# Kernel optimization log

Hardware: AMD Instinct MI355X
Metric: run time of the kernel (lower is better)

The kernel has to match this reference:

```python
import jax, jax.numpy as jnp
import numpy as np

ACT_BIT = 3
W_BIT = 2


def fake_quant(x, bits):
    """Symmetric uniform fake-quantization to `bits` bits (dequantized values)."""
    qmax = float((1 << (bits - 1)) - 1)
    scale = jnp.max(jnp.abs(x)) / qmax
    scale = jnp.where(scale == 0, jnp.ones_like(scale), scale)
    return jnp.clip(jnp.round(x / scale), -qmax, qmax) * scale


def setup_inputs() -> dict:
    key = jax.random.key(0)
    kA, kX, kWi, kWo = jax.random.split(key, 4)
    N, D_IN, D_H, D_OUT = 8192, 128, 64, 16
    A = jax.random.normal(kA, (N, N), dtype=jnp.float32)       # dense subgraph adjacency (binarized inside)
    X = jax.random.normal(kX, (N, D_IN), dtype=jnp.float32)    # node features
    W_in = jax.random.normal(kWi, (D_IN, D_H), dtype=jnp.float32)
    W_out = jax.random.normal(kWo, (D_H, D_OUT), dtype=jnp.float32)
    return {"A": A, "X": X, "W_in": W_in, "W_out": W_out}


def reference(A, X, W_in, W_out):
    # QGTC GCNConv_Qnt: A quantized to 1 bit, activations to act_bit, weights to w_bit.
    Aq = (A > 0).astype(A.dtype)                 # 1-bit adjacency (bit_qnt(A, 1))
    Xq = fake_quant(X, ACT_BIT)                  # X_Qnt
    Wi = fake_quant(W_in, W_BIT)                 # weight_Qnt
    Wo = fake_quant(W_out, W_BIT)
    # Layer 1: mm_v1(X, W_in) then mm_v1(A, .) with output re-quantized to act_bit
    h = Aq @ (Xq @ Wi)                           # [N, D_H]
    hq = fake_quant(h, ACT_BIT)
    # Layer 2 (output layer)
    out = Aq @ (hq @ Wo)                         # [N, D_OUT]
    return out
```

## Files before the change

### kernel.cpp

```cpp
#include <hip/hip_runtime.h>

#define NN 8192
#define DIN 128
#define DH 64
#define DOUT 16
#define KS 8

typedef _Float16 half8 __attribute__((ext_vector_type(8)));
typedef float f32x4 __attribute__((ext_vector_type(4)));

#define OFF_SC    0u
#define OFF_PART  256u
#define OFF_YT    65536u
#define OFF_RT    1114112u
#define OFF_HF    1376256u
#define OFF_BITS  3473408u
#define OFF_P1    11862016u

__device__ __forceinline__ int permk(int k) {
  int e = k & 255;
  return (k & ~255) | (((e & 3) << 6) | (e >> 2));
}

__device__ __forceinline__ float getscale(const unsigned* sc, int idx, float qmax) {
  float s = __uint_as_float(sc[idx]) / qmax;
  return (s == 0.0f) ? 1.0f : s;
}

__device__ __forceinline__ half8 expand8(unsigned bb) {
  uint4 w;
  w.x = ((bb & 1u)  ? 0x3C00u : 0u) | ((bb & 2u)   ? 0x3C000000u : 0u);
  w.y = ((bb & 4u)  ? 0x3C00u : 0u) | ((bb & 8u)   ? 0x3C000000u : 0u);
  w.z = ((bb & 16u) ? 0x3C00u : 0u) | ((bb & 32u)  ? 0x3C000000u : 0u);
  w.w = ((bb & 64u) ? 0x3C00u : 0u) | ((bb & 128u) ? 0x3C000000u : 0u);
  return __builtin_bit_cast(half8, w);
}

__global__ __launch_bounds__(256) void k_scalesbits(const float* __restrict__ A,
                                                    const float* __restrict__ X,
                                                    const float* __restrict__ Wi,
                                                    const float* __restrict__ Wo,
                                                    unsigned char* __restrict__ bits,
                                                    unsigned* part, unsigned* sc) {
  const int t = threadIdx.x, bx = blockIdx.x;
  if (bx < 4096) {
    const int lane = t & 63, warp = t >> 6;
    const size_t wbase = ((size_t)bx * 4 + warp) * 4096;
    const float4* ap = (const float4*)(A + wbase) + lane;
    unsigned char* bp = bits + (wbase >> 3);
#pragma unroll
    for (int g = 0; g < 16; ++g) {
      float4 v = ap[g * 64];
      unsigned long long m0 = __ballot(v.x > 0.0f);
      unsigned long long m1 = __ballot(v.y > 0.0f);
      unsigned long long m2 = __ballot(v.z > 0.0f);
      unsigned long long m3 = __ballot(v.w > 0.0f);
      unsigned long long lo = (lane & 1) ? m1 : m0;
      unsigned long long hi = (lane & 1) ? m3 : m2;
      unsigned long long word = (lane & 2) ? hi : lo;
      if (lane < 4) *(unsigned long long*)(bp + g * 32 + lane * 8) = word;
    }
    return;
  }
  __shared__ float red[256];
  const int b = bx - 4096;
  float m = 0.0f;
  if (b < 240) {
    for (int i = b * 256 + t; i < NN * DIN; i += 240 * 256) m = fmaxf(m, fabsf(X[i]));
  } else if (b == 240) {
    for (int i = t; i < DIN * DH; i += 256) m = fmaxf(m, fabsf(Wi[i]));
    if (t == 0) sc[3] = 0u;
  } else {
    for (int i = t; i < DH * DOUT; i += 256) m = fmaxf(m, fabsf(Wo[i]));
  }
  red[t] = m; __syncthreads();
  for (int s = 128; s > 0; s >>= 1) {
    if (t < s) red[t] = fmaxf(red[t], red[t + s]);
    __syncthreads();
  }
  if (t == 0) part[b] = __float_as_uint(red[0]);
}

__global__ __launch_bounds__(256) void k_Y(const float* __restrict__ X,
                                           const float* __restrict__ Wi,
                                           const unsigned* __restrict__ part,
                                           unsigned* sc,
                                           _Float16* __restrict__ Yb) {
  __shared__ float red[256];
  __shared__ float Xs[8][129];
  __shared__ float Ws[DIN][DH];
  const int t = threadIdx.x;
  red[t] = (t < 240) ? __uint_as_float(part[t]) : 0.0f;
  __syncthreads();
  for (int s = 128; s > 0; s >>= 1) {
    if (t < s) red[t] = fmaxf(red[t], red[t + s]);
    __syncthreads();
  }
  float sxraw = red[0];
  float sx = sxraw / 3.0f; sx = (sx == 0.0f) ? 1.0f : sx;
  float swi = __uint_as_float(part[240]); swi = (swi == 0.0f) ? 1.0f : swi;
  if (blockIdx.x == 0 && t == 0) sc[0] = __float_as_uint(sxraw);
  const int k0 = blockIdx.x * 8;
  __syncthreads();
  for (int i = t; i < 8 * DIN; i += 256) {
    int r = i >> 7, c = i & 127;
    float q = rintf(X[(size_t)(k0 + r) * DIN + c] / sx);
    Xs[r][c] = fminf(fmaxf(q, -3.0f), 3.0f);
  }
  for (int i = t; i < DIN * DH; i += 256) {
    float q = rintf(Wi[i] / swi);
    Ws[i >> 6][i & 63] = fminf(fmaxf(q, -1.0f), 1.0f);
  }
  __syncthreads();
  const int r = t & 7, jp = t >> 3, j = jp * 2;
  float a0 = 0.0f, a1 = 0.0f;
  for (int n = 0; n < DIN; ++n) {
    float xv = Xs[r][n];
    a0 = fmaf(xv, Ws[n][j], a0);
    a1 = fmaf(xv, Ws[n][j + 1], a1);
  }
  const int kp = permk(k0 + r);
  const size_t base = (size_t)(kp >> 3) * 512 + (size_t)j * 8 + (kp & 7);
  Yb[base]     = (_Float16)a0;
  Yb[base + 8] = (_Float16)a1;
}

__global__ __launch_bounds__(256) void k_gemm1(const unsigned char* __restrict__ bits,
                                               const _Float16* __restrict__ Yb,
                                               float* __restrict__ P1) {
  __shared__ __align__(16) char Ls[65536];
  const int t = threadIdx.x, lane = t & 63, warp = t >> 6;
  const int row0 = blockIdx.x * 256;
  const int split = blockIdx.y;
  const int l15 = lane & 15, lq = lane >> 4;
  const int sh8 = lq * 8;

  f32x4 acc[4][4] = {};
  const char* ysrc = (const char*)Yb + (size_t)split * 131072;
  const unsigned char* bbase = bits + split * 128;

  for (int half = 0; half < 2; ++half) {
    __syncthreads();
    {
      const uint4* src = (const uint4*)(ysrc + half * 65536) + t;
      uint4* dst = (uint4*)Ls + t;
#pragma unroll
      for (int p = 0; p < 16; ++p) dst[p * 256] = src[p * 256];
    }
    __syncthreads();
#pragma unroll
    for (int it = 0; it < 8; ++it) {
      uint2 w[4];
#pragma unroll
      for (int rt = 0; rt < 4; ++rt)
        w[rt] = *(const uint2*)(bbase +
                 (size_t)(row0 + warp * 64 + rt * 16 + l15) * 1024 + half * 64 + it * 8);
#pragma unroll
      for (int kk = 0; kk < 2; ++kk) {
        half8 bf[4];
#pragma unroll
        for (int nt = 0; nt < 4; ++nt)
          bf[nt] = *(const half8*)(&Ls[(it * 8 + kk * 4 + lq) * 1024 + (nt * 16 + l15) * 16]);
#pragma unroll
        for (int rt = 0; rt < 4; ++rt) {
          half8 af = expand8(((kk ? w[rt].y : w[rt].x) >> sh8) & 0xffu);
#pragma unroll
          for (int nt = 0; nt < 4; ++nt)
            acc[rt][nt] = __builtin_amdgcn_mfma_f32_16x16x32_f16(af, bf[nt], acc[rt][nt], 0, 0, 0);
        }
      }
    }
  }
  const int r4 = lq * 4;
#pragma unroll
  for (int rt = 0; rt < 4; ++rt) {
#pragma unroll
    for (int nt = 0; nt < 4; ++nt) {
#pragma unroll
      for (int i = 0; i < 4; ++i) {
        int rr = row0 + warp * 64 + rt * 16 + r4 + i;
        int cc = nt * 16 + l15;
        P1[((size_t)split * NN + rr) * DH + cc] = acc[rt][nt][i];
      }
    }
  }
}

__global__ __launch_bounds__(256) void k_h2(const float* __restrict__ P1,
                                            const unsigned* __restrict__ part,
                                            unsigned* sc, float* __restrict__ hf) {
  float sx = getscale(sc, 0, 3.0f);
  float swi = __uint_as_float(part[240]); swi = (swi == 0.0f) ? 1.0f : swi;
  float sxw = sx * swi;
  int idx = blockIdx.x * 256 + threadIdx.x;
  const float4* p = (const float4*)P1;
  float4 s = {0, 0, 0, 0};
#pragma unroll
  for (int sp = 0; sp < KS; ++sp) {
    float4 v = p[(size_t)sp * (NN * DH / 4) + idx];
    s.x += v.x; s.y += v.y; s.z += v.z; s.w += v.w;
  }
  s.x *= sxw; s.y *= sxw; s.z *= sxw; s.w *= sxw;
  ((float4*)hf)[idx] = s;
  float m = fmaxf(fmaxf(fabsf(s.x), fabsf(s.y)), fmaxf(fabsf(s.z), fabsf(s.w)));
  __shared__ float red[256];
  red[threadIdx.x] = m; __syncthreads();
  for (int st = 128; st > 0; st >>= 1) {
    if (threadIdx.x < st) red[threadIdx.x] = fmaxf(red[threadIdx.x], red[threadIdx.x + st]);
    __syncthreads();
  }
  if (threadIdx.x == 0) atomicMax(&sc[3], __float_as_uint(red[0]));
}

__global__ __launch_bounds__(256) void k_R(const float* __restrict__ hf,
                                           const float* __restrict__ Wo,
                                           const unsigned* __restrict__ part,
                                           const unsigned* __restrict__ sc,
                                           _Float16* __restrict__ RT) {
  __shared__ float WoS[DH][DOUT];
  float sh = getscale(sc, 3, 3.0f);
  float swo = __uint_as_float(part[241]); swo = (swo == 0.0f) ? 1.0f : swo;
  int t = threadIdx.x;
  for (int i = t; i < DH * DOUT; i += 256) {
    float q = rintf(Wo[i] / swo);
    WoS[i >> 4][i & 15] = fminf(fmaxf(q, -1.0f), 1.0f);
  }
  __syncthreads();
  int i = blockIdx.x * 16 + (t & 15), j = t >> 4;
  const float4* hp = (const float4*)(hf + (size_t)i * DH);
  float acc = 0.0f;
#pragma unroll 4
  for (int nb = 0; nb < 16; ++nb) {
    float4 h4 = hp[nb];
    float q;
    q = fminf(fmaxf(rintf(h4.x / sh), -3.0f), 3.0f); acc = fmaf(q, WoS[nb * 4 + 0][j], acc);
    q = fminf(fmaxf(rintf(h4.y / sh), -3.0f), 3.0f); acc = fmaf(q, WoS[nb * 4 + 1][j], acc);
    q = fminf(fmaxf(rintf(h4.z / sh), -3.0f), 3.0f); acc = fmaf(q, WoS[nb * 4 + 2][j], acc);
    q = fminf(fmaxf(rintf(h4.w / sh), -3.0f), 3.0f); acc = fmaf(q, WoS[nb * 4 + 3][j], acc);
  }
  RT[(size_t)j * NN + permk(i)] = (_Float16)acc;
}

__global__ __launch_bounds__(256) void k_gemm2(const unsigned char* __restrict__ bits,
                                               const _Float16* __restrict__ RT,
                                               const unsigned* __restrict__ part,
                                               const unsigned* __restrict__ sc,
                                               float* __restrict__ out) {
  __shared__ float red2[3][16][16];
  const int t = threadIdx.x, lane = t & 63, warp = t >> 6;
  const int row0 = blockIdx.x * 16;
  const int l15 = lane & 15, lq = lane >> 4;
  const int sh8 = lq * 8;

  const unsigned char* brow = bits + (size_t)(row0 + l15) * 1024 + warp * 256;
  const _Float16* rrow = RT + (size_t)l15 * NN + warp * 2048 + lq * 8;

  f32x4 acc = {};
#pragma unroll 8
  for (int it = 0; it < 32; ++it) {
    uint2 w = *(const uint2*)(brow + it * 8);
#pragma unroll
    for (int kk = 0; kk < 2; ++kk) {
      half8 af = expand8(((kk ? w.y : w.x) >> sh8) & 0xffu);
      half8 bf = *(const half8*)(rrow + it * 64 + kk * 32);
      acc = __builtin_amdgcn_mfma_f32_16x16x32_f16(af, bf, acc, 0, 0, 0);
    }
  }
  if (warp > 0) {
#pragma unroll
    for (int i = 0; i < 4; ++i) red2[warp - 1][lq * 4 + i][l15] = acc[i];
  }
  __syncthreads();
  if (warp == 0) {
    float sh = getscale(sc, 3, 3.0f);
    float swo = __uint_as_float(part[241]); swo = (swo == 0.0f) ? 1.0f : swo;
    float s = sh * swo;
#pragma unroll
    for (int i = 0; i < 4; ++i) {
      int r = lq * 4 + i;
      float v = acc[i] + red2[0][r][l15] + red2[1][r][l15] + red2[2][r][l15];
      out[(size_t)(row0 + r) * DOUT + l15] = v * s;
    }
  }
}

extern "C" void kernel_launch(void* const* d_in, const int* in_sizes, int n_in,
                              void* d_out, int out_size, void* d_ws, size_t ws_size,
                              hipStream_t stream) {
  const float* A  = (const float*)d_in[0];
  const float* X  = (const float*)d_in[1];
  const float* Wi = (const float*)d_in[2];
  const float* Wo = (const float*)d_in[3];
  char* ws = (char*)d_ws;
  unsigned* sc        = (unsigned*)(ws + OFF_SC);
  unsigned* part      = (unsigned*)(ws + OFF_PART);
  _Float16* Yb        = (_Float16*)(ws + OFF_YT);
  _Float16* RT        = (_Float16*)(ws + OFF_RT);
  float* hf           = (float*)(ws + OFF_HF);
  unsigned char* bits = (unsigned char*)(ws + OFF_BITS);
  float* P1           = (float*)(ws + OFF_P1);
  float* out          = (float*)d_out;

  k_scalesbits<<<4338, 256, 0, stream>>>(A, X, Wi, Wo, bits, part, sc);
  k_Y<<<1024, 256, 0, stream>>>(X, Wi, part, sc, Yb);
  k_gemm1<<<dim3(NN / 256, KS), 256, 0, stream>>>(bits, Yb, P1);
  k_h2<<<NN * DH / 1024, 256, 0, stream>>>(P1, part, sc, hf);
  k_R<<<NN / 16, 256, 0, stream>>>(hf, Wo, part, sc, RT);
  k_gemm2<<<NN / 16, 256, 0, stream>>>(bits, RT, part, sc, out);
}
```

Measured before the change: 127.0 us.

## Restructure pipeline into uniform 512-block kernels with atomic-free scale reductions

Rewrites all six kernels to run on a fixed grid of 512 blocks. The adjacency-binarization blocks now loop over several chunks instead of launching thousands of small blocks. The first adjacency GEMM doubles its K-split and reads Y fragments straight from global/L2 instead of staging them through 64KB of LDS. The atomicMax on the hidden-layer max is replaced by per-block partials that each consumer re-reduces, and the combined scale factors are folded into the final output. This is meant to cut launch and occupancy overhead and LDS pressure, at the cost of doubling the partial-sum buffer traffic and repeating small reductions in every block.

```diff
diff --git a/kernel.cpp b/kernel.cpp
--- a/kernel.cpp
+++ b/kernel.cpp
@@ -4,14 +4,14 @@
 #define DIN 128
 #define DH 64
 #define DOUT 16
-#define KS 8
+#define KS 16
 
 typedef _Float16 half8 __attribute__((ext_vector_type(8)));
 typedef float f32x4 __attribute__((ext_vector_type(4)));
 
-#define OFF_SC    0u
-#define OFF_PART  256u
-#define OFF_YT    65536u
+#define OFF_PART  0u
+#define OFF_PART2 2048u
+#define OFF_YB    65536u
 #define OFF_RT    1114112u
 #define OFF_HF    1376256u
 #define OFF_BITS  3473408u
@@ -22,10 +22,7 @@
   return (k & ~255) | (((e & 3) << 6) | (e >> 2));
 }
 
-__device__ __forceinline__ float getscale(const unsigned* sc, int idx, float qmax) {
-  float s = __uint_as_float(sc[idx]) / qmax;
-  return (s == 0.0f) ? 1.0f : s;
-}
+__device__ __forceinline__ float guard(float s) { return (s == 0.0f) ? 1.0f : s; }
 
 __device__ __forceinline__ half8 expand8(unsigned bb) {
   uint4 w;
@@ -36,16 +33,17 @@
   return __builtin_bit_cast(half8, w);
 }
 
-__global__ __launch_bounds__(256) void k_scalesbits(const float* __restrict__ A,
-                                                    const float* __restrict__ X,
-                                                    const float* __restrict__ Wi,
-                                                    const float* __restrict__ Wo,
-                                                    unsigned char* __restrict__ bits,
-                                                    unsigned* part, unsigned* sc) {
-  const int t = threadIdx.x, bx = blockIdx.x;
-  if (bx < 4096) {
-    const int lane = t & 63, warp = t >> 6;
-    const size_t wbase = ((size_t)bx * 4 + warp) * 4096;
+__global__ __launch_bounds__(256) void k_f0(const float* __restrict__ A,
+                                            const float* __restrict__ X,
+                                            const float* __restrict__ Wi,
+                                            const float* __restrict__ Wo,
+                                            unsigned char* __restrict__ bits,
+                                            unsigned* __restrict__ part) {
+  __shared__ float red0[256];
+  const int t = threadIdx.x, bid = blockIdx.x;
+  const int lane = t & 63, warp = t >> 6;
+  for (int c = 0; c < 8; ++c) {
+    const size_t wbase = (((size_t)bid * 4 + warp) * 8 + c) * 4096;
     const float4* ap = (const float4*)(A + wbase) + lane;
     unsigned char* bp = bits + (wbase >> 3);
 #pragma unroll
@@ -60,49 +58,43 @@
       unsigned long long word = (lane & 2) ? hi : lo;
       if (lane < 4) *(unsigned long long*)(bp + g * 32 + lane * 8) = word;
     }
-    return;
-  }
-  __shared__ float red[256];
-  const int b = bx - 4096;
+  }
   float m = 0.0f;
-  if (b < 240) {
-    for (int i = b * 256 + t; i < NN * DIN; i += 240 * 256) m = fmaxf(m, fabsf(X[i]));
-  } else if (b == 240) {
+  if (bid < 240) {
+    for (int i = bid * 256 + t; i < NN * DIN; i += 240 * 256) m = fmaxf(m, fabsf(X[i]));
+  } else if (bid == 240) {
     for (int i = t; i < DIN * DH; i += 256) m = fmaxf(m, fabsf(Wi[i]));
-    if (t == 0) sc[3] = 0u;
-  } else {
+  } else if (bid == 241) {
     for (int i = t; i < DH * DOUT; i += 256) m = fmaxf(m, fabsf(Wo[i]));
   }
-  red[t] = m; __syncthreads();
+  if (bid < 242) {
+    red0[t] = m; __syncthreads();
+    for (int s = 128; s > 0; s >>= 1) {
+      if (t < s) red0[t] = fmaxf(red0[t], red0[t + s]);
+      __syncthreads();
+    }
+    if (t == 0) part[bid] = __float_as_uint(red0[0]);
+  }
+}
+
+__global__ __launch_bounds__(256) void k_f1(const float* __restrict__ X,
+                                            const float* __restrict__ Wi,
+                                            const unsigned* __restrict__ part,
+                                            _Float16* __restrict__ Yb) {
+  __shared__ float Xs[16][129];
+  __shared__ float Ws[DIN][DH];
+  __shared__ float red1[256];
+  const int t = threadIdx.x, bid = blockIdx.x;
+  red1[t] = (t < 240) ? __uint_as_float(part[t]) : 0.0f;
+  __syncthreads();
   for (int s = 128; s > 0; s >>= 1) {
-    if (t < s) red[t] = fmaxf(red[t], red[t + s]);
-    __syncthreads();
-  }
-  if (t == 0) part[b] = __float_as_uint(red[0]);
-}
-
-__global__ __launch_bounds__(256) void k_Y(const float* __restrict__ X,
-                                           const float* __restrict__ Wi,
-                                           const unsigned* __restrict__ part,
-                                           unsigned* sc,
-                                           _Float16* __restrict__ Yb) {
-  __shared__ float red[256];
-  __shared__ float Xs[8][129];
-  __shared__ float Ws[DIN][DH];
-  const int t = threadIdx.x;
-  red[t] = (t < 240) ? __uint_as_float(part[t]) : 0.0f;
-  __syncthreads();
-  for (int s = 128; s > 0; s >>= 1) {
-    if (t < s) red[t] = fmaxf(red[t], red[t + s]);
-    __syncthreads();
-  }
-  float sxraw = red[0];
-  float sx = sxraw / 3.0f; sx = (sx == 0.0f) ? 1.0f : sx;
-  float swi = __uint_as_float(part[240]); swi = (swi == 0.0f) ? 1.0f : swi;
-  if (blockIdx.x == 0 && t == 0) sc[0] = __float_as_uint(sxraw);
-  const int k0 = blockIdx.x * 8;
-  __syncthreads();
-  for (int i = t; i < 8 * DIN; i += 256) {
+    if (t < s) red1[t] = fmaxf(red1[t], red1[t + s]);
+    __syncthreads();
+  }
+  const float sx = guard(red1[0] / 3.0f);
+  const float swi = guard(__uint_as_float(part[240]));
+  const int k0 = bid * 16;
+  for (int i = t; i < 16 * DIN; i += 256) {
     int r = i >> 7, c = i & 127;
     float q = rintf(X[(size_t)(k0 + r) * DIN + c] / sx);
     Xs[r][c] = fminf(fmaxf(q, -3.0f), 3.0f);
@@ -112,87 +104,69 @@
     Ws[i >> 6][i & 63] = fminf(fmaxf(q, -1.0f), 1.0f);
   }
   __syncthreads();
-  const int r = t & 7, jp = t >> 3, j = jp * 2;
-  float a0 = 0.0f, a1 = 0.0f;
-  for (int n = 0; n < DIN; ++n) {
-    float xv = Xs[r][n];
-    a0 = fmaf(xv, Ws[n][j], a0);
-    a1 = fmaf(xv, Ws[n][j + 1], a1);
-  }
-  const int kp = permk(k0 + r);
-  const size_t base = (size_t)(kp >> 3) * 512 + (size_t)j * 8 + (kp & 7);
-  Yb[base]     = (_Float16)a0;
-  Yb[base + 8] = (_Float16)a1;
-}
-
-__global__ __launch_bounds__(256) void k_gemm1(const unsigned char* __restrict__ bits,
-                                               const _Float16* __restrict__ Yb,
-                                               float* __restrict__ P1) {
-  __shared__ __align__(16) char Ls[65536];
-  const int t = threadIdx.x, lane = t & 63, warp = t >> 6;
-  const int row0 = blockIdx.x * 256;
-  const int split = blockIdx.y;
+#pragma unroll
+  for (int rg = 0; rg < 2; ++rg) {
+    const int r = rg * 8 + (t & 7), j = (t >> 3) * 2;
+    float a0 = 0.0f, a1 = 0.0f;
+    for (int n = 0; n < DIN; ++n) {
+      float xv = Xs[r][n];
+      a0 = fmaf(xv, Ws[n][j], a0);
+      a1 = fmaf(xv, Ws[n][j + 1], a1);
+    }
+    const int kp = permk(k0 + r);
+    const size_t base = (size_t)(kp >> 3) * 512 + (size_t)j * 8 + (kp & 7);
+    Yb[base]     = (_Float16)a0;
+    Yb[base + 8] = (_Float16)a1;
+  }
+}
+
+__global__ __launch_bounds__(256) void k_f2(const unsigned char* __restrict__ bits,
+                                            const _Float16* __restrict__ Yb,
+                                            float* __restrict__ P1) {
+  const int t = threadIdx.x, bid = blockIdx.x;
+  const int lane = t & 63, warp = t >> 6;
   const int l15 = lane & 15, lq = lane >> 4;
-  const int sh8 = lq * 8;
-
+  const int rowblk = bid >> 4, split = bid & 15;
+  const int row0 = rowblk * 256 + warp * 64;
   f32x4 acc[4][4] = {};
-  const char* ysrc = (const char*)Yb + (size_t)split * 131072;
-  const unsigned char* bbase = bits + split * 128;
-
-  for (int half = 0; half < 2; ++half) {
-    __syncthreads();
-    {
-      const uint4* src = (const uint4*)(ysrc + half * 65536) + t;
-      uint4* dst = (uint4*)Ls + t;
-#pragma unroll
-      for (int p = 0; p < 16; ++p) dst[p * 256] = src[p * 256];
-    }
-    __syncthreads();
-#pragma unroll
-    for (int it = 0; it < 8; ++it) {
-      uint2 w[4];
-#pragma unroll
-      for (int rt = 0; rt < 4; ++rt)
-        w[rt] = *(const uint2*)(bbase +
-                 (size_t)(row0 + warp * 64 + rt * 16 + l15) * 1024 + half * 64 + it * 8);
-#pragma unroll
-      for (int kk = 0; kk < 2; ++kk) {
-        half8 bf[4];
+  const unsigned char* b0 = bits + (size_t)(row0 + l15) * 1024 + split * 64;
+#pragma unroll
+  for (int it = 0; it < 8; ++it) {
+    uint2 w[4];
+#pragma unroll
+    for (int rt = 0; rt < 4; ++rt)
+      w[rt] = *(const uint2*)(b0 + (size_t)rt * 16384 + it * 8);
+#pragma unroll
+    for (int kk = 0; kk < 2; ++kk) {
+      const _Float16* yb = Yb + (size_t)(split * 64 + it * 8 + kk * 4 + lq) * 512 + (size_t)l15 * 8;
+      half8 bf[4];
+#pragma unroll
+      for (int nt = 0; nt < 4; ++nt) bf[nt] = *(const half8*)(yb + nt * 128);
+#pragma unroll
+      for (int rt = 0; rt < 4; ++rt) {
+        half8 af = expand8(((kk ? w[rt].y : w[rt].x) >> (lq * 8)) & 0xffu);
 #pragma unroll
         for (int nt = 0; nt < 4; ++nt)
-          bf[nt] = *(const half8*)(&Ls[(it * 8 + kk * 4 + lq) * 1024 + (nt * 16 + l15) * 16]);
-#pragma unroll
-        for (int rt = 0; rt < 4; ++rt) {
-          half8 af = expand8(((kk ? w[rt].y : w[rt].x) >> sh8) & 0xffu);
-#pragma unroll
-          for (int nt = 0; nt < 4; ++nt)
-            acc[rt][nt] = __builtin_amdgcn_mfma_f32_16x16x32_f16(af, bf[nt], acc[rt][nt], 0, 0, 0);
-        }
+          acc[rt][nt] = __builtin_amdgcn_mfma_f32_16x16x32_f16(af, bf[nt], acc[rt][nt], 0, 0, 0);
       }
     }
   }
   const int r4 = lq * 4;
 #pragma unroll
-  for (int rt = 0; rt < 4; ++rt) {
-#pragma unroll
-    for (int nt = 0; nt < 4; ++nt) {
-#pragma unroll
-      for (int i = 0; i < 4; ++i) {
-        int rr = row0 + warp * 64 + rt * 16 + r4 + i;
-        int cc = nt * 16 + l15;
-        P1[((size_t)split * NN + rr) * DH + cc] = acc[rt][nt][i];
-      }
-    }
-  }
-}
-
-__global__ __launch_bounds__(256) void k_h2(const float* __restrict__ P1,
-                                            const unsigned* __restrict__ part,
-                                            unsigned* sc, float* __restrict__ hf) {
-  float sx = getscale(sc, 0, 3.0f);
-  float swi = __uint_as_float(part[240]); swi = (swi == 0.0f) ? 1.0f : swi;
-  float sxw = sx * swi;
-  int idx = blockIdx.x * 256 + threadIdx.x;
+  for (int rt = 0; rt < 4; ++rt)
+#pragma unroll
+    for (int nt = 0; nt < 4; ++nt)
+#pragma unroll
+      for (int i = 0; i < 4; ++i)
+        P1[((size_t)split * NN + row0 + rt * 16 + r4 + i) * DH + nt * 16 + l15] = acc[rt][nt][i];
+}
+
+__global__ __launch_bounds__(256) void k_f3(const float* __restrict__ P1,
+                                            float* __restrict__ hf,
+                                            unsigned* __restrict__ part2) {
+  __shared__ float red3[256];
+  const int t = threadIdx.x, bid = blockIdx.x;
+  const int idx = bid * 256 + t;
   const float4* p = (const float4*)P1;
   float4 s = {0, 0, 0, 0};
 #pragma unroll
@@ -200,86 +174,108 @@
     float4 v = p[(size_t)sp * (NN * DH / 4) + idx];
     s.x += v.x; s.y += v.y; s.z += v.z; s.w += v.w;
   }
-  s.x *= sxw; s.y *= sxw; s.z *= sxw; s.w *= sxw;
   ((float4*)hf)[idx] = s;
   float m = fmaxf(fmaxf(fabsf(s.x), fabsf(s.y)), fmaxf(fabsf(s.z), fabsf(s.w)));
-  __shared__ float red[256];
-  red[threadIdx.x] = m; __syncthreads();
+  red3[t] = m; __syncthreads();
   for (int st = 128; st > 0; st >>= 1) {
-    if (threadIdx.x < st) red[threadIdx.x] = fmaxf(red[threadIdx.x], red[threadIdx.x + st]);
-    __syncthreads();
-  }
-  if (threadIdx.x == 0) atomicMax(&sc[3], __float_as_uint(red[0]));
-}
-
-__global__ __launch_bounds__(256) void k_R(const float* __restrict__ hf,
-                                           const float* __restrict__ Wo,
-                                           const unsigned* __restrict__ part,
-                                           const unsigned* __restrict__ sc,
-                                           _Float16* __restrict__ RT) {
+    if (t < st) red3[t] = fmaxf(red3[t], red3[t + st]);
+    __syncthreads();
+  }
+  if (t == 0) part2[bid] = __float_as_uint(red3[0]);
+}
+
+__global__ __launch_bounds__(256) void k_f4(const float* __restrict__ hf,
+                                            const float* __restrict__ Wo,
+                                            const unsigned* __restrict__ part,
+                                            const unsigned* __restrict__ part2,
+                                            _Float16* __restrict__ RT) {
   __shared__ float WoS[DH][DOUT];
-  float sh = getscale(sc, 3, 3.0f);
-  float swo = __uint_as_float(part[241]); swo = (swo == 0.0f) ? 1.0f : swo;
-  int t = threadIdx.x;
+  __shared__ float red4[256];
+  const int t = threadIdx.x, bid = blockIdx.x;
+  red4[t] = fmaxf(__uint_as_float(part2[t]), __uint_as_float(part2[t + 256]));
+  __syncthreads();
+  for (int s = 128; s > 0; s >>= 1) {
+    if (t < s) red4[t] = fmaxf(red4[t], red4[t + s]);
+    __syncthreads();
+  }
+  const float shi = guard(red4[0] / 3.0f);
+  const float swo = guard(__uint_as_float(part[241]));
   for (int i = t; i < DH * DOUT; i += 256) {
     float q = rintf(Wo[i] / swo);
     WoS[i >> 4][i & 15] = fminf(fmaxf(q, -1.0f), 1.0f);
   }
   __syncthreads();
-  int i = blockIdx.x * 16 + (t & 15), j = t >> 4;
+  const int i = bid * 16 + (t & 15), j = t >> 4;
   const float4* hp = (const float4*)(hf + (size_t)i * DH);
   float acc = 0.0f;
 #pragma unroll 4
   for (int nb = 0; nb < 16; ++nb) {
     float4 h4 = hp[nb];
     float q;
-    q = fminf(fmaxf(rintf(h4.x / sh), -3.0f), 3.0f); acc = fmaf(q, WoS[nb * 4 + 0][j], acc);
-    q = fminf(fmaxf(rintf(h4.y / sh), -3.0f), 3.0f); acc = fmaf(q, WoS[nb * 4 + 1][j], acc);
-    q = fminf(fmaxf(rintf(h4.z / sh), -3.0f), 3.0f); acc = fmaf(q, WoS[nb * 4 + 2][j], acc);
-    q = fminf(fmaxf(rintf(h4.w / sh), -3.0f), 3.0f); acc = fmaf(q, WoS[nb * 4 + 3][j], acc);
+    q = fminf(fmaxf(rintf(h4.x / shi), -3.0f), 3.0f); acc = fmaf(q, WoS[nb * 4 + 0][j], acc);
+    q = fminf(fmaxf(rintf(h4.y / shi), -3.0f), 3.0f); acc = fmaf(q, WoS[nb * 4 + 1][j], acc);
+    q = fminf(fmaxf(rintf(h4.z / shi), -3.0f), 3.0f); acc = fmaf(q, WoS[nb * 4 + 2][j], acc);
+    q = fminf(fmaxf(rintf(h4.w / shi), -3.0f), 3.0f); acc = fmaf(q, WoS[nb * 4 + 3][j], acc);
   }
   RT[(size_t)j * NN + permk(i)] = (_Float16)acc;
 }
 
-__global__ __launch_bounds__(256) void k_gemm2(const unsigned char* __restrict__ bits,
-                                               const _Float16* __restrict__ RT,
-                                               const unsigned* __restrict__ part,
-                                               const unsigned* __restrict__ sc,
-                                               float* __restrict__ out) {
-  __shared__ float red2[3][16][16];
-  const int t = threadIdx.x, lane = t & 63, warp = t >> 6;
-  const int row0 = blockIdx.x * 16;
+__global__ __launch_bounds__(256) void k_f5(const unsigned char* __restrict__ bits,
+                                            const _Float16* __restrict__ RT,
+                                            const unsigned* __restrict__ part,
+                                            const unsigned* __restrict__ part2,
+                                            float* __restrict__ out) {
+  __shared__ float redP[256];
+  __shared__ float red2s[3][16][16];
+  const int t = threadIdx.x, bid = blockIdx.x;
+  redP[t] = (t < 240) ? __uint_as_float(part[t]) : 0.0f;
+  __syncthreads();
+  for (int s = 128; s > 0; s >>= 1) {
+    if (t < s) redP[t] = fmaxf(redP[t], redP[t + s]);
+    __syncthreads();
+  }
+  const float sxraw = redP[0];
+  __syncthreads();
+  redP[t] = fmaxf(__uint_as_float(part2[t]), __uint_as_float(part2[t + 256]));
+  __syncthreads();
+  for (int s = 128; s > 0; s >>= 1) {
+    if (t < s) redP[t] = fmaxf(redP[t], redP[t + s]);
+    __syncthreads();
+  }
+  const float maxint = redP[0];
+  const float swi = guard(__uint_as_float(part[240]));
+  const float swo = guard(__uint_as_float(part[241]));
+  const float sx = guard(sxraw / 3.0f);
+  const float shF = (maxint == 0.0f) ? 1.0f : (sx * swi) * (maxint / 3.0f);
+  const float sfin = shF * swo;
+
+  const int lane = t & 63, warp = t >> 6;
   const int l15 = lane & 15, lq = lane >> 4;
-  const int sh8 = lq * 8;
-
+  const int row0 = bid * 16;
   const unsigned char* brow = bits + (size_t)(row0 + l15) * 1024 + warp * 256;
   const _Float16* rrow = RT + (size_t)l15 * NN + warp * 2048 + lq * 8;
-
   f32x4 acc = {};
 #pragma unroll 8
   for (int it = 0; it < 32; ++it) {
     uint2 w = *(const uint2*)(brow + it * 8);
 #pragma unroll
     for (int kk = 0; kk < 2; ++kk) {
-      half8 af = expand8(((kk ? w.y : w.x) >> sh8) & 0xffu);
+      half8 af = expand8(((kk ? w.y : w.x) >> (lq * 8)) & 0xffu);
       half8 bf = *(const half8*)(rrow + it * 64 + kk * 32);
       acc = __builtin_amdgcn_mfma_f32_16x16x32_f16(af, bf, acc, 0, 0, 0);
     }
   }
   if (warp > 0) {
 #pragma unroll
-    for (int i = 0; i < 4; ++i) red2[warp - 1][lq * 4 + i][l15] = acc[i];
+    for (int i = 0; i < 4; ++i) red2s[warp - 1][lq * 4 + i][l15] = acc[i];
   }
   __syncthreads();
   if (warp == 0) {
-    float sh = getscale(sc, 3, 3.0f);
-    float swo = __uint_as_float(part[241]); swo = (swo == 0.0f) ? 1.0f : swo;
-    float s = sh * swo;
 #pragma unroll
     for (int i = 0; i < 4; ++i) {
       int r = lq * 4 + i;
-      float v = acc[i] + red2[0][r][l15] + red2[1][r][l15] + red2[2][r][l15];
-      out[(size_t)(row0 + r) * DOUT + l15] = v * s;
+      float v = acc[i] + red2s[0][r][l15] + red2s[1][r][l15] + red2s[2][r][l15];
+      out[(size_t)(row0 + r) * DOUT + l15] = v * sfin;
     }
   }
 }
@@ -292,19 +288,19 @@
   const float* Wi = (const float*)d_in[2];
   const float* Wo = (const float*)d_in[3];
   char* ws = (char*)d_ws;
-  unsigned* sc        = (unsigned*)(ws + OFF_SC);
   unsigned* part      = (unsigned*)(ws + OFF_PART);
-  _Float16* Yb        = (_Float16*)(ws + OFF_YT);
+  unsigned* part2     = (unsigned*)(ws + OFF_PART2);
+  _Float16* Yb        = (_Float16*)(ws + OFF_YB);
   _Float16* RT        = (_Float16*)(ws + OFF_RT);
   float* hf           = (float*)(ws + OFF_HF);
   unsigned char* bits = (unsigned char*)(ws + OFF_BITS);
   float* P1           = (float*)(ws + OFF_P1);
-  float* out          = (float*)d_out;
-
-  k_scalesbits<<<4338, 256, 0, stream>>>(A, X, Wi, Wo, bits, part, sc);
-  k_Y<<<1024, 256, 0, stream>>>(X, Wi, part, sc, Yb);
-  k_gemm1<<<dim3(NN / 256, KS), 256, 0, stream>>>(bits, Yb, P1);
-  k_h2<<<NN * DH / 1024, 256, 0, stream>>>(P1, part, sc, hf);
-  k_R<<<NN / 16, 256, 0, stream>>>(hf, Wo, part, sc, RT);
-  k_gemm2<<<NN / 16, 256, 0, stream>>>(bits, RT, part, sc, out);
-}
+  float* outp         = (float*)d_out;
+
+  k_f0<<<512, 256, 0, stream>>>(A, X, Wi, Wo, bits, part);
+  k_f1<<<512, 256, 0, stream>>>(X, Wi, part, Yb);
+  k_f2<<<512, 256, 0, stream>>>(bits, Yb, P1);
+  k_f3<<<512, 256, 0, stream>>>(P1, hf, part2);
+  k_f4<<<512, 256, 0, stream>>>(hf, Wo, part, part2, RT);
+  k_f5<<<512, 256, 0, stream>>>(bits, RT, part, part2, outp);
+}
```

Result: slower. 157.2 us (+23.7%).
